# Kernel optimization log

Measured on AMD Instinct MI355X. Metric: run time of the kernel, lower is better.

The kernel has to match this reference:

```python
import jax, jax.numpy as jnp
import numpy as np

ALPHA = 300.0  # attractor strength (exp variant: exp(-alpha*|dx|^gamma)*dx, gamma=2)


def setup_inputs() -> dict:
    key = jax.random.key(0)
    k0, k1, k2, k3 = jax.random.split(key, 4)
    n, c, h, w = 4, 256, 128, 128
    mlp_dim, n_attractors, n_bins = 128, 16, 64
    x = jax.random.normal(k0, (n, c, h, w), jnp.float32)
    b_prev = jax.random.uniform(k1, (n, n_bins, h, w), jnp.float32)  # bin centers
    w1 = jax.random.normal(k2, (mlp_dim, c), jnp.float32) * 0.02
    b1 = jnp.zeros((mlp_dim,), jnp.float32)
    w2 = jax.random.normal(k3, (n_attractors, mlp_dim), jnp.float32) * 0.02
    b2 = jnp.zeros((n_attractors,), jnp.float32)
    return {"x": x, "b_prev": b_prev, "w1": w1, "b1": b1, "w2": w2, "b2": b2}


def reference(x, b_prev, w1, b1, w2, b2):
    # 1x1 conv MLP head: Conv2d(c->mlp) -> ReLU -> Conv2d(mlp->n_attractors) -> Softplus
    hfeat = jax.nn.relu(jnp.einsum('nchw,oc->nohw', x, w1) + b1[None, :, None, None])
    A = jax.nn.softplus(jnp.einsum('nchw,oc->nohw', hfeat, w2) + b2[None, :, None, None])
    # b_prev interpolated to (h, w) == identity here (same spatial size)
    b_centers = b_prev
    # dx: [n, n_attractors, n_bins, h, w]
    dx = A[:, :, None, :, :] - b_centers[:, None, :, :, :]
    # exp attractor with gamma=2: exp(-alpha*dx^2) * dx, summed over attractors ('sum' kind)
    delta_c = jnp.sum(jnp.exp(-ALPHA * dx * dx) * dx, axis=1)
    b_new_centers = b_centers + delta_c
    return (b_new_centers, b_new_centers)
```

## Files before the change

kernel.cpp:

```cpp
#include <hip/hip_runtime.h>
#include <hip/hip_bf16.h>
#include <stdint.h>


#define HW 16384
#define ALPHA 300.0f

typedef short bf16x8_t __attribute__((ext_vector_type(8)));
typedef float f32x4_t __attribute__((ext_vector_type(4)));
typedef unsigned int u32x4_t __attribute__((ext_vector_type(4)));

__device__ __forceinline__ unsigned short f2bf(float f) {
  unsigned int u = __builtin_bit_cast(unsigned int, f);
  u += 0x7fffu + ((u >> 16) & 1u);
  return (unsigned short)(u >> 16);
}
__device__ __forceinline__ unsigned int pack2(float a, float b) {
  return (unsigned int)f2bf(a) | ((unsigned int)f2bf(b) << 16);
}

__global__ void zoed_prep(const float* __restrict__ w1,
                          const float* __restrict__ w2,
                          unsigned short* __restrict__ blob) {
  int i = blockIdx.x * 256 + threadIdx.x;
  if (i < 32768) {
    int o = i >> 8, c = i & 255;
    float v = w1[i];
    int idx = (c >> 5) * 4096 + o * 32 + ((((c >> 3) & 3) ^ (o & 3)) << 3) + (c & 7);
    blob[idx] = f2bf(v);
  } else {
    int i2 = i - 32768;
    int a = i2 >> 7, o = i2 & 127;
    float v = w2[i2];
    int idx = 32768 + (o >> 5) * 512 + a * 32 + ((((o >> 3) & 3) ^ (a & 3)) << 3) + (o & 7);
    blob[idx] = f2bf(v);
  }
}

__global__ __launch_bounds__(256, 4) void zoed_fused(
    const float* __restrict__ x, const float* __restrict__ bprev,
    const float* __restrict__ b1, const float* __restrict__ b2,
    const unsigned short* __restrict__ wblob, float* __restrict__ out) {
  __shared__ __align__(16) char smem[20480];
  char* hid = smem;
  char* Albuf = smem + 16384;

  const int t = threadIdx.x;
  const int lane = t & 63;
  const int l15 = lane & 15;
  const int quad = lane >> 4;
  const int wv = t >> 6;
  const int wm = wv & 1;
  const int wn = wv >> 1;
  const int sw = ((quad ^ (lane & 3)) << 4);

  const int blk = blockIdx.x;
  const int n = blk >> 8;
  const int p0 = (blk & 255) << 6;

  const int sp = t & 63;
  const int sg = t >> 6;

  const float* xsbase = x + (size_t)(n * 256 + sg * 8) * HW + p0 + sp;
  float xr[4][8];
#pragma unroll
  for (int c = 0; c < 4; c++)
#pragma unroll
    for (int j = 0; j < 8; j++)
      xr[c][j] = xsbase[(size_t)(c * 32 + j) * HW];

  const char* wbase = (const char*)wblob + (wm * 64 + l15) * 64 + sw;
  bf16x8_t afn[4];
#pragma unroll
  for (int tm = 0; tm < 4; tm++)
    afn[tm] = *(const bf16x8_t*)(wbase + tm * 1024);

  f32x4_t acc[4][2];
#pragma unroll
  for (int i = 0; i < 4; i++)
#pragma unroll
    for (int j = 0; j < 2; j++) acc[i][j] = (f32x4_t){0.f, 0.f, 0.f, 0.f};

#pragma unroll
  for (int kb = 0; kb < 8; ++kb) {
    char* xb = smem + (kb & 1) * 4096;
    bf16x8_t afc[4];
#pragma unroll
    for (int tm = 0; tm < 4; tm++) afc[tm] = afn[tm];
    if (kb < 7) {
#pragma unroll
      for (int tm = 0; tm < 4; tm++)
        afn[tm] = *(const bf16x8_t*)(wbase + (kb + 1) * 8192 + tm * 1024);
    }
    {
      u32x4_t v = {pack2(xr[kb & 3][0], xr[kb & 3][1]),
                   pack2(xr[kb & 3][2], xr[kb & 3][3]),
                   pack2(xr[kb & 3][4], xr[kb & 3][5]),
                   pack2(xr[kb & 3][6], xr[kb & 3][7])};
      *(u32x4_t*)(xb + sp * 64 + ((sg ^ (sp & 3)) << 4)) = v;
    }
    if (kb < 4) {
#pragma unroll
      for (int j = 0; j < 8; j++)
        xr[kb & 3][j] = xsbase[(size_t)((kb + 4) * 32 + j) * HW];
    }
    __syncthreads();
    bf16x8_t bfm[2];
#pragma unroll
    for (int tn = 0; tn < 2; tn++)
      bfm[tn] = *(const bf16x8_t*)(xb + (wn * 32 + tn * 16 + l15) * 64 + sw);
#pragma unroll
    for (int tm = 0; tm < 4; tm++)
#pragma unroll
      for (int tn = 0; tn < 2; tn++)
        acc[tm][tn] = __builtin_amdgcn_mfma_f32_16x16x32_bf16(
            afc[tm], bfm[tn], acc[tm][tn], 0, 0, 0);
  }

  const int ap = t & 63;
  const int grp = t >> 6;
  size_t obase = (size_t)n * 64 * HW + (size_t)(grp * 16) * HW + (size_t)(p0 + ap);
  const float* bp = bprev + obase;
  float bpr[16];
#pragma unroll
  for (int b = 0; b < 16; b++) bpr[b] = bp[(size_t)b * HW];
  bf16x8_t a2[4];
#pragma unroll
  for (int kc = 0; kc < 4; kc++)
    a2[kc] = *(const bf16x8_t*)((const char*)wblob + 65536 + kc * 1024 +
                                l15 * 64 + sw);

  __syncthreads();
#pragma unroll
  for (int tm = 0; tm < 4; tm++) {
    f32x4_t b1v = *(const f32x4_t*)(b1 + wm * 64 + tm * 16 + quad * 4);
    int kc = wm * 2 + (tm >> 1);
    int g = (tm & 1) * 2 + (quad >> 1);
    int off8 = (quad & 1) * 8;
#pragma unroll
    for (int tn = 0; tn < 2; tn++) {
      f32x4_t h = acc[tm][tn] + b1v;
      h[0] = fmaxf(h[0], 0.f);
      h[1] = fmaxf(h[1], 0.f);
      h[2] = fmaxf(h[2], 0.f);
      h[3] = fmaxf(h[3], 0.f);
      int prow = wn * 32 + tn * 16 + l15;
      unsigned int* dst = (unsigned int*)(hid + kc * 4096 + prow * 64 +
                                          ((g ^ (prow & 3)) << 4) + off8);
      dst[0] = pack2(h[0], h[1]);
      dst[1] = pack2(h[2], h[3]);
    }
  }
  __syncthreads();
  {
    f32x4_t acc2 = (f32x4_t){0.f, 0.f, 0.f, 0.f};
    const int prow = wv * 16 + l15;
#pragma unroll
    for (int kc = 0; kc < 4; kc++) {
      bf16x8_t bh = *(const bf16x8_t*)(hid + kc * 4096 + prow * 64 + sw);
      acc2 = __builtin_amdgcn_mfma_f32_16x16x32_bf16(a2[kc], bh, acc2, 0, 0, 0);
    }
    f32x4_t b2v = *(const f32x4_t*)(b2 + quad * 4);
    f32x4_t z = acc2 + b2v;
    f32x4_t spv;
#pragma unroll
    for (int r = 0; r < 4; r++) {
      float zz = z[r];
      spv[r] = fmaxf(zz, 0.f) + log1pf(__expf(-fabsf(zz)));
    }
    *(f32x4_t*)(Albuf + prow * 64 + ((quad ^ (prow & 3)) << 4)) = spv;
  }
  __syncthreads();
  {
    float Av[16];
#pragma unroll
    for (int q = 0; q < 4; q++) {
      f32x4_t v = *(const f32x4_t*)(Albuf + ap * 64 + ((q ^ (ap & 3)) << 4));
      Av[q * 4 + 0] = v[0];
      Av[q * 4 + 1] = v[1];
      Av[q * 4 + 2] = v[2];
      Av[q * 4 + 3] = v[3];
    }
    float* o1 = out + obase;
    float* o2 = out + (size_t)4 * 64 * HW + obase;
#pragma unroll
    for (int b = 0; b < 16; b++) {
      float c = bpr[b];
      float d0 = 0.f, d1 = 0.f;
#pragma unroll
      for (int a = 0; a < 8; a++) {
        float dx = Av[a] - c;
        float e = __expf(dx * dx * -ALPHA);
        d0 = fmaf(e, dx, d0);
      }
#pragma unroll
      for (int a = 8; a < 16; a++) {
        float dx = Av[a] - c;
        float e = __expf(dx * dx * -ALPHA);
        d1 = fmaf(e, dx, d1);
      }
      float r = c + (d0 + d1);
      __builtin_nontemporal_store(r, o1 + (size_t)b * HW);
      __builtin_nontemporal_store(r, o2 + (size_t)b * HW);
    }
  }
}

extern "C" void kernel_launch(void* const* d_in, const int* in_sizes, int n_in,
                              void* d_out, int out_size, void* d_ws,
                              size_t ws_size, hipStream_t stream) {
  const float* x = (const float*)d_in[0];
  const float* bprev = (const float*)d_in[1];
  const float* w1 = (const float*)d_in[2];
  const float* b1 = (const float*)d_in[3];
  const float* w2 = (const float*)d_in[4];
  const float* b2 = (const float*)d_in[5];
  float* outp = (float*)d_out;
  unsigned short* blob = (unsigned short*)d_ws;

  zoed_prep<<<136, 256, 0, stream>>>(w1, w2, blob);
  zoed_fused<<<1024, 256, 0, stream>>>(x, bprev, b1, b2, blob, outp);
}
```

Baseline: 132.3 us.

## Split fused MLP and attractor stages into separate kernels

The single fused kernel becomes two launches. A GEMM kernel computes the softplus attractor values and writes them into the second output copy, which serves as scratch space. A new 512-thread attractor kernel then reads them back together with b_prev and writes both outputs. The goal is lower register pressure and better occupancy for each phase, at the cost of an extra kernel launch and an extra round trip of the attractor tensor through global memory. Correctness depends on every read of the scratch region within a block finishing before its writes overwrite it.

```diff
diff --git a/kernel.cpp b/kernel.cpp
--- a/kernel.cpp
+++ b/kernel.cpp
@@ -37,13 +37,12 @@
   }
 }
 
-__global__ __launch_bounds__(256, 4) void zoed_fused(
-    const float* __restrict__ x, const float* __restrict__ bprev,
-    const float* __restrict__ b1, const float* __restrict__ b2,
-    const unsigned short* __restrict__ wblob, float* __restrict__ out) {
-  __shared__ __align__(16) char smem[20480];
+__global__ __launch_bounds__(256, 4) void zoed_gemm(
+    const float* __restrict__ x, const float* __restrict__ b1,
+    const float* __restrict__ b2, const unsigned short* __restrict__ wblob,
+    float* __restrict__ out) {
+  __shared__ __align__(16) char smem[16384];
   char* hid = smem;
-  char* Albuf = smem + 16384;
 
   const int t = threadIdx.x;
   const int lane = t & 63;
@@ -117,13 +116,6 @@
             afc[tm], bfm[tn], acc[tm][tn], 0, 0, 0);
   }
 
-  const int ap = t & 63;
-  const int grp = t >> 6;
-  size_t obase = (size_t)n * 64 * HW + (size_t)(grp * 16) * HW + (size_t)(p0 + ap);
-  const float* bp = bprev + obase;
-  float bpr[16];
-#pragma unroll
-  for (int b = 0; b < 16; b++) bpr[b] = bp[(size_t)b * HW];
   bf16x8_t a2[4];
 #pragma unroll
   for (int kc = 0; kc < 4; kc++)
@@ -162,47 +154,59 @@
     }
     f32x4_t b2v = *(const f32x4_t*)(b2 + quad * 4);
     f32x4_t z = acc2 + b2v;
-    f32x4_t spv;
+    float* Adst = out + (size_t)(256 + n * 64 + quad * 4) * HW + p0 + prow;
 #pragma unroll
     for (int r = 0; r < 4; r++) {
       float zz = z[r];
-      spv[r] = fmaxf(zz, 0.f) + log1pf(__expf(-fabsf(zz)));
-    }
-    *(f32x4_t*)(Albuf + prow * 64 + ((quad ^ (prow & 3)) << 4)) = spv;
-  }
+      float spv = fmaxf(zz, 0.f) + log1pf(__expf(-fabsf(zz)));
+      Adst[(size_t)r * HW] = spv;
+    }
+  }
+}
+
+__global__ __launch_bounds__(512, 8) void zoed_attr(
+    const float* __restrict__ bprev, float* __restrict__ out) {
+  const int t = threadIdx.x;
+  const int px = t & 63;
+  const int grp = t >> 6;
+  const int blk = blockIdx.x;
+  const int n = blk >> 8;
+  const int p0 = (blk & 255) << 6;
+
+  const float* Abase = out + (size_t)(256 + n * 64) * HW + p0 + px;
+  float Av[16];
+#pragma unroll
+  for (int a = 0; a < 16; a++) Av[a] = Abase[(size_t)a * HW];
+
+  size_t obase = (size_t)(n * 64 + grp * 8) * HW + p0 + px;
+  const float* bp = bprev + obase;
+  float bpr[8];
+#pragma unroll
+  for (int b = 0; b < 8; b++) bpr[b] = bp[(size_t)b * HW];
+
   __syncthreads();
-  {
-    float Av[16];
-#pragma unroll
-    for (int q = 0; q < 4; q++) {
-      f32x4_t v = *(const f32x4_t*)(Albuf + ap * 64 + ((q ^ (ap & 3)) << 4));
-      Av[q * 4 + 0] = v[0];
-      Av[q * 4 + 1] = v[1];
-      Av[q * 4 + 2] = v[2];
-      Av[q * 4 + 3] = v[3];
-    }
-    float* o1 = out + obase;
-    float* o2 = out + (size_t)4 * 64 * HW + obase;
-#pragma unroll
-    for (int b = 0; b < 16; b++) {
-      float c = bpr[b];
-      float d0 = 0.f, d1 = 0.f;
-#pragma unroll
-      for (int a = 0; a < 8; a++) {
-        float dx = Av[a] - c;
-        float e = __expf(dx * dx * -ALPHA);
-        d0 = fmaf(e, dx, d0);
-      }
-#pragma unroll
-      for (int a = 8; a < 16; a++) {
-        float dx = Av[a] - c;
-        float e = __expf(dx * dx * -ALPHA);
-        d1 = fmaf(e, dx, d1);
-      }
-      float r = c + (d0 + d1);
-      __builtin_nontemporal_store(r, o1 + (size_t)b * HW);
-      __builtin_nontemporal_store(r, o2 + (size_t)b * HW);
-    }
+
+  float* o1 = out + obase;
+  float* o2 = out + (size_t)256 * HW + obase;
+#pragma unroll
+  for (int b = 0; b < 8; b++) {
+    float c = bpr[b];
+    float d0 = 0.f, d1 = 0.f;
+#pragma unroll
+    for (int a = 0; a < 8; a++) {
+      float dx = Av[a] - c;
+      float e = __expf(dx * dx * -ALPHA);
+      d0 = fmaf(e, dx, d0);
+    }
+#pragma unroll
+    for (int a = 8; a < 16; a++) {
+      float dx = Av[a] - c;
+      float e = __expf(dx * dx * -ALPHA);
+      d1 = fmaf(e, dx, d1);
+    }
+    float r = c + (d0 + d1);
+    __builtin_nontemporal_store(r, o1 + (size_t)b * HW);
+    __builtin_nontemporal_store(r, o2 + (size_t)b * HW);
   }
 }
 
@@ -219,5 +223,6 @@
   unsigned short* blob = (unsigned short*)d_ws;
 
   zoed_prep<<<136, 256, 0, stream>>>(w1, w2, blob);
-  zoed_fused<<<1024, 256, 0, stream>>>(x, bprev, b1, b2, blob, outp);
-}
+  zoed_gemm<<<1024, 256, 0, stream>>>(x, b1, b2, blob, outp);
+  zoed_attr<<<1024, 512, 0, stream>>>(bprev, outp);
+}
```

New measurement: 136.4 us. +3.1%, slower.

## Make each wave own 16 pixels end-to-end, dropping block barriers

Applied to the files above, without the earlier changes.

Restructures the fused kernel so each wavefront computes all 128 hidden channels for its own 16 pixels. The x tile now feeds the MFMA B operand straight from registers instead of going through shared memory, and all __syncthreads are removed; shared memory is only used per wave for the hidden and attractor transposes. The b_prev loads are interleaved into the K loop to hide their latency. The cost is that every wave now reloads all W1 fragments from global/L2 each k-step (8 per step instead of 4) and holds more accumulator registers, which may hurt occupancy.

```diff
diff --git a/kernel.cpp b/kernel.cpp
--- a/kernel.cpp
+++ b/kernel.cpp
@@ -41,125 +41,100 @@
     const float* __restrict__ x, const float* __restrict__ bprev,
     const float* __restrict__ b1, const float* __restrict__ b2,
     const unsigned short* __restrict__ wblob, float* __restrict__ out) {
-  __shared__ __align__(16) char smem[20480];
-  char* hid = smem;
-  char* Albuf = smem + 16384;
+  __shared__ __align__(16) char smem[21504];
 
   const int t = threadIdx.x;
   const int lane = t & 63;
   const int l15 = lane & 15;
   const int quad = lane >> 4;
   const int wv = t >> 6;
-  const int wm = wv & 1;
-  const int wn = wv >> 1;
-  const int sw = ((quad ^ (lane & 3)) << 4);
+  const int sw = ((quad ^ (l15 & 3)) << 4);
 
   const int blk = blockIdx.x;
   const int n = blk >> 8;
-  const int p0 = (blk & 255) << 6;
+  const int p0 = ((blk & 255) << 6) + wv * 16;
 
-  const int sp = t & 63;
-  const int sg = t >> 6;
+  char* hid = smem + wv * 4096;
+  char* Ab = smem + 16384 + wv * 1280;
 
-  const float* xsbase = x + (size_t)(n * 256 + sg * 8) * HW + p0 + sp;
+  const float* xb = x + (size_t)(n * 256 + quad * 8) * HW + p0 + l15;
+
   float xr[4][8];
 #pragma unroll
-  for (int c = 0; c < 4; c++)
+  for (int c = 0; c < 3; c++)
 #pragma unroll
     for (int j = 0; j < 8; j++)
-      xr[c][j] = xsbase[(size_t)(c * 32 + j) * HW];
+      xr[c][j] = xb[(size_t)(c * 32 + j) * HW];
 
-  const char* wbase = (const char*)wblob + (wm * 64 + l15) * 64 + sw;
-  bf16x8_t afn[4];
+  size_t obase = (size_t)(n * 64 + quad * 16) * HW + p0 + l15;
+  const float* bp = bprev + obase;
+  float bpr[16];
+
+  f32x4_t acc[8];
 #pragma unroll
-  for (int tm = 0; tm < 4; tm++)
-    afn[tm] = *(const bf16x8_t*)(wbase + tm * 1024);
+  for (int i = 0; i < 8; i++) acc[i] = (f32x4_t){0.f, 0.f, 0.f, 0.f};
 
-  f32x4_t acc[4][2];
-#pragma unroll
-  for (int i = 0; i < 4; i++)
-#pragma unroll
-    for (int j = 0; j < 2; j++) acc[i][j] = (f32x4_t){0.f, 0.f, 0.f, 0.f};
+  const char* wb = (const char*)wblob + l15 * 64 + sw;
 
 #pragma unroll
   for (int kb = 0; kb < 8; ++kb) {
-    char* xb = smem + (kb & 1) * 4096;
-    bf16x8_t afc[4];
+    bf16x8_t af[8];
 #pragma unroll
-    for (int tm = 0; tm < 4; tm++) afc[tm] = afn[tm];
-    if (kb < 7) {
-#pragma unroll
-      for (int tm = 0; tm < 4; tm++)
-        afn[tm] = *(const bf16x8_t*)(wbase + (kb + 1) * 8192 + tm * 1024);
-    }
-    {
-      u32x4_t v = {pack2(xr[kb & 3][0], xr[kb & 3][1]),
-                   pack2(xr[kb & 3][2], xr[kb & 3][3]),
-                   pack2(xr[kb & 3][4], xr[kb & 3][5]),
-                   pack2(xr[kb & 3][6], xr[kb & 3][7])};
-      *(u32x4_t*)(xb + sp * 64 + ((sg ^ (sp & 3)) << 4)) = v;
-    }
-    if (kb < 4) {
+    for (int tm = 0; tm < 8; tm++)
+      af[tm] = *(const bf16x8_t*)(wb + kb * 8192 + tm * 1024);
+    if (kb < 5) {
 #pragma unroll
       for (int j = 0; j < 8; j++)
-        xr[kb & 3][j] = xsbase[(size_t)((kb + 4) * 32 + j) * HW];
+        xr[(kb + 3) & 3][j] = xb[(size_t)((kb + 3) * 32 + j) * HW];
     }
-    __syncthreads();
-    bf16x8_t bfm[2];
+    if (kb == 5) {
 #pragma unroll
-    for (int tn = 0; tn < 2; tn++)
-      bfm[tn] = *(const bf16x8_t*)(xb + (wn * 32 + tn * 16 + l15) * 64 + sw);
+      for (int b = 0; b < 8; b++) bpr[b] = bp[(size_t)b * HW];
+    }
+    if (kb == 6) {
 #pragma unroll
-    for (int tm = 0; tm < 4; tm++)
+      for (int b = 8; b < 16; b++) bpr[b] = bp[(size_t)b * HW];
+    }
+    u32x4_t v = {pack2(xr[kb & 3][0], xr[kb & 3][1]),
+                 pack2(xr[kb & 3][2], xr[kb & 3][3]),
+                 pack2(xr[kb & 3][4], xr[kb & 3][5]),
+                 pack2(xr[kb & 3][6], xr[kb & 3][7])};
+    bf16x8_t bfm = __builtin_bit_cast(bf16x8_t, v);
 #pragma unroll
-      for (int tn = 0; tn < 2; tn++)
-        acc[tm][tn] = __builtin_amdgcn_mfma_f32_16x16x32_bf16(
-            afc[tm], bfm[tn], acc[tm][tn], 0, 0, 0);
+    for (int tm = 0; tm < 8; tm++)
+      acc[tm] = __builtin_amdgcn_mfma_f32_16x16x32_bf16(af[tm], bfm, acc[tm],
+                                                        0, 0, 0);
   }
 
-  const int ap = t & 63;
-  const int grp = t >> 6;
-  size_t obase = (size_t)n * 64 * HW + (size_t)(grp * 16) * HW + (size_t)(p0 + ap);
-  const float* bp = bprev + obase;
-  float bpr[16];
-#pragma unroll
-  for (int b = 0; b < 16; b++) bpr[b] = bp[(size_t)b * HW];
   bf16x8_t a2[4];
 #pragma unroll
   for (int kc = 0; kc < 4; kc++)
     a2[kc] = *(const bf16x8_t*)((const char*)wblob + 65536 + kc * 1024 +
                                 l15 * 64 + sw);
 
-  __syncthreads();
 #pragma unroll
-  for (int tm = 0; tm < 4; tm++) {
-    f32x4_t b1v = *(const f32x4_t*)(b1 + wm * 64 + tm * 16 + quad * 4);
-    int kc = wm * 2 + (tm >> 1);
+  for (int tm = 0; tm < 8; tm++) {
+    f32x4_t b1v = *(const f32x4_t*)(b1 + tm * 16 + quad * 4);
+    f32x4_t h = acc[tm] + b1v;
+    h[0] = fmaxf(h[0], 0.f);
+    h[1] = fmaxf(h[1], 0.f);
+    h[2] = fmaxf(h[2], 0.f);
+    h[3] = fmaxf(h[3], 0.f);
+    int kc = tm >> 1;
     int g = (tm & 1) * 2 + (quad >> 1);
     int off8 = (quad & 1) * 8;
+    unsigned int* dst = (unsigned int*)(hid + kc * 1024 + l15 * 64 +
+                                        ((g ^ (l15 & 3)) << 4) + off8);
+    dst[0] = pack2(h[0], h[1]);
+    dst[1] = pack2(h[2], h[3]);
+  }
+  f32x4_t acc2 = (f32x4_t){0.f, 0.f, 0.f, 0.f};
 #pragma unroll
-    for (int tn = 0; tn < 2; tn++) {
-      f32x4_t h = acc[tm][tn] + b1v;
-      h[0] = fmaxf(h[0], 0.f);
-      h[1] = fmaxf(h[1], 0.f);
-      h[2] = fmaxf(h[2], 0.f);
-      h[3] = fmaxf(h[3], 0.f);
-      int prow = wn * 32 + tn * 16 + l15;
-      unsigned int* dst = (unsigned int*)(hid + kc * 4096 + prow * 64 +
-                                          ((g ^ (prow & 3)) << 4) + off8);
-      dst[0] = pack2(h[0], h[1]);
-      dst[1] = pack2(h[2], h[3]);
-    }
+  for (int kc = 0; kc < 4; kc++) {
+    bf16x8_t bh = *(const bf16x8_t*)(hid + kc * 1024 + l15 * 64 + sw);
+    acc2 = __builtin_amdgcn_mfma_f32_16x16x32_bf16(a2[kc], bh, acc2, 0, 0, 0);
   }
-  __syncthreads();
   {
-    f32x4_t acc2 = (f32x4_t){0.f, 0.f, 0.f, 0.f};
-    const int prow = wv * 16 + l15;
-#pragma unroll
-    for (int kc = 0; kc < 4; kc++) {
-      bf16x8_t bh = *(const bf16x8_t*)(hid + kc * 4096 + prow * 64 + sw);
-      acc2 = __builtin_amdgcn_mfma_f32_16x16x32_bf16(a2[kc], bh, acc2, 0, 0, 0);
-    }
     f32x4_t b2v = *(const f32x4_t*)(b2 + quad * 4);
     f32x4_t z = acc2 + b2v;
     f32x4_t spv;
@@ -168,41 +143,38 @@
       float zz = z[r];
       spv[r] = fmaxf(zz, 0.f) + log1pf(__expf(-fabsf(zz)));
     }
-    *(f32x4_t*)(Albuf + prow * 64 + ((quad ^ (prow & 3)) << 4)) = spv;
+    *(f32x4_t*)(Ab + l15 * 80 + quad * 16) = spv;
   }
-  __syncthreads();
-  {
-    float Av[16];
+  float Av[16];
 #pragma unroll
-    for (int q = 0; q < 4; q++) {
-      f32x4_t v = *(const f32x4_t*)(Albuf + ap * 64 + ((q ^ (ap & 3)) << 4));
-      Av[q * 4 + 0] = v[0];
-      Av[q * 4 + 1] = v[1];
-      Av[q * 4 + 2] = v[2];
-      Av[q * 4 + 3] = v[3];
+  for (int r = 0; r < 4; r++) {
+    f32x4_t v = *(const f32x4_t*)(Ab + l15 * 80 + r * 16);
+    Av[r * 4 + 0] = v[0];
+    Av[r * 4 + 1] = v[1];
+    Av[r * 4 + 2] = v[2];
+    Av[r * 4 + 3] = v[3];
+  }
+  float* o1 = out + obase;
+  float* o2 = o1 + (size_t)256 * HW;
+#pragma unroll
+  for (int b = 0; b < 16; b++) {
+    float c = bpr[b];
+    float d0 = 0.f, d1 = 0.f;
+#pragma unroll
+    for (int a = 0; a < 8; a++) {
+      float dx = Av[a] - c;
+      float e = __expf(dx * dx * -ALPHA);
+      d0 = fmaf(e, dx, d0);
     }
-    float* o1 = out + obase;
-    float* o2 = out + (size_t)4 * 64 * HW + obase;
 #pragma unroll
-    for (int b = 0; b < 16; b++) {
-      float c = bpr[b];
-      float d0 = 0.f, d1 = 0.f;
-#pragma unroll
-      for (int a = 0; a < 8; a++) {
-        float dx = Av[a] - c;
-        float e = __expf(dx * dx * -ALPHA);
-        d0 = fmaf(e, dx, d0);
-      }
-#pragma unroll
-      for (int a = 8; a < 16; a++) {
-        float dx = Av[a] - c;
-        float e = __expf(dx * dx * -ALPHA);
-        d1 = fmaf(e, dx, d1);
-      }
-      float r = c + (d0 + d1);
-      __builtin_nontemporal_store(r, o1 + (size_t)b * HW);
-      __builtin_nontemporal_store(r, o2 + (size_t)b * HW);
+    for (int a = 8; a < 16; a++) {
+      float dx = Av[a] - c;
+      float e = __expf(dx * dx * -ALPHA);
+      d1 = fmaf(e, dx, d1);
     }
+    float r = c + (d0 + d1);
+    __builtin_nontemporal_store(r, o1 + (size_t)b * HW);
+    __builtin_nontemporal_store(r, o2 + (size_t)b * HW);
   }
 }
 
```

After: 145.8 us. +10.2%, slower.
